# Performance work log

Measured on AMD Instinct MI355X. Metric: run time of the kernel, lower is better.

The kernel has to match this reference:

```python
import jax, jax.numpy as jnp
import numpy as np

EPS = 1e-5  # BatchNorm eps

B, LMAX = 64, 512
N_IN, N_OUT = 128, 256
LENGTHS = np.array([128 if i % 2 == 0 else 384 for i in range(B)], dtype=np.int64)  # sum = 16384
M = int(LENGTHS.sum())


def _bn(x, gamma, beta, mean, var):
    # eval-mode BatchNorm over channel (last) dim; x: [M, C]
    return (x - mean) * (gamma / jnp.sqrt(var + EPS)) + beta


def _aggregate(x, ld, am):
    # x: [M, N] ragged-concatenated node features; ld: [B] lengths; am: [B, L, L]
    # Equivalent to per-graph am[j,:l,:l] @ x_block, vectorized via zero-padding:
    # padded columns of am hit zero rows of x, and garbage rows are never gathered.
    Bn, L, _ = am.shape
    gid = jnp.repeat(jnp.arange(Bn), ld, total_repeat_length=x.shape[0])      # [M] graph id per node
    offs = jnp.concatenate([jnp.zeros((1,), ld.dtype), jnp.cumsum(ld)[:-1]])  # [B] start offsets
    pos = jnp.arange(x.shape[0]) - offs[gid]                                   # [M] within-graph position
    padded = jnp.zeros((Bn, L, x.shape[1]), x.dtype).at[gid, pos].set(x)       # [B, L, N]
    out = jnp.einsum('blm,bmn->bln', am, padded)                               # batched adjacency matmul
    return out[gid, pos]                                                       # back to ragged [M, N]


def setup_inputs() -> dict:
    key = jax.random.key(0)
    ks = jax.random.split(key, 12)
    x = jax.random.normal(ks[0], (M, N_IN, 1, 1), dtype=jnp.float32)
    ld = jnp.asarray(LENGTHS)
    am = jax.random.normal(ks[1], (B, LMAX, LMAX), dtype=jnp.float32)

    def lin_bn(kw, kb, cin, cout):
        W = jax.random.normal(kw, (cout, cin), dtype=jnp.float32) / np.sqrt(cin)
        b = jax.random.normal(kb, (cout,), dtype=jnp.float32) * 0.01
        kg, kbt, km, kv = jax.random.split(jax.random.fold_in(kw, 7), 4)
        gamma = 1.0 + 0.1 * jax.random.normal(kg, (cout,), dtype=jnp.float32)
        beta = 0.1 * jax.random.normal(kbt, (cout,), dtype=jnp.float32)
        mean = 0.1 * jax.random.normal(km, (cout,), dtype=jnp.float32)
        var = 0.5 + jax.random.uniform(kv, (cout,), dtype=jnp.float32)
        return W, b, gamma, beta, mean, var

    Wl, bl, gl, betal, ml, vl = lin_bn(ks[2], ks[3], N_IN, N_OUT)   # residual 1x1 conv + BN
    W1, b1, g1, beta1, m1, v1 = lin_bn(ks[4], ks[5], N_IN, N_IN)    # graph conv layer 1
    W2, b2, g2, beta2, m2, v2 = lin_bn(ks[6], ks[7], N_IN, N_OUT)   # graph conv layer 2
    return {
        'x': x, 'ld': ld, 'am': am,
        'Wl': Wl, 'bl': bl, 'gl': gl, 'betal': betal, 'ml': ml, 'vl': vl,
        'W1': W1, 'b1': b1, 'g1': g1, 'beta1': beta1, 'm1': m1, 'v1': v1,
        'W2': W2, 'b2': b2, 'g2': g2, 'beta2': beta2, 'm2': m2, 'v2': v2,
    }


def reference(x, ld, am,
              Wl, bl, gl, betal, ml, vl,
              W1, b1, g1, beta1, m1, v1,
              W2, b2, g2, beta2, m2, v2):
    xf = x.reshape(x.shape[0], x.shape[1])  # squeeze [M, N, 1, 1] -> [M, N]
    # residual branch (input_size != output_size): 1x1 conv + BN
    residual = _bn(xf @ Wl.T + bl, gl, betal, ml, vl)
    # graph conv layer 1: aggregate -> conv1x1 -> BN -> ReLU (dropout inactive in eval)
    h = _aggregate(xf, ld, am)
    h = jax.nn.relu(_bn(h @ W1.T + b1, g1, beta1, m1, v1))
    # graph conv layer 2: aggregate -> conv1x1 -> BN
    h = _aggregate(h, ld, am)
    h = _bn(h @ W2.T + b2, g2, beta2, m2, v2)
    out = jax.nn.leaky_relu(h + residual, negative_slope=0.01)
    return out[:, :, None, None]  # [M, N_out, 1, 1]
```

## Files before the change

kernel.cpp:

```cpp
#include <hip/hip_runtime.h>

#define EPS 1e-5f

typedef __attribute__((ext_vector_type(4))) float f32x4;
typedef __attribute__((ext_vector_type(8))) _Float16 f16x8;
typedef __attribute__((ext_vector_type(4))) _Float16 f16x4;

__device__ __forceinline__ int tidx(int r, int k, int K) {
    return (r >> 4) * (K << 4) + ((k >> 5) << 9) + ((r & 15) << 5) + (((k & 31) >> 3) << 3) + (k & 7);
}

#define MFMA16(a, b, c) __builtin_amdgcn_mfma_f32_16x16x32_f16(a, b, c, 0, 0, 0)

__device__ __forceinline__ void slot_map(int s, int& g, int& r0) {
    int c = s >> 6, j = s & 63;
    if (j < 48) { g = c * 8 + 2 * (j / 12) + 1; r0 = (j % 12) << 5; }
    else        { int jj = j - 48; g = c * 8 + 2 * (jj / 4); r0 = (jj % 4) << 5; }
}

__global__ __launch_bounds__(256) void prep_conv_kernel(
    const int* __restrict__ ld, const float* __restrict__ am,
    const float* __restrict__ Wl, const float* __restrict__ bl,
    const float* __restrict__ gl, const float* __restrict__ betal,
    const float* __restrict__ ml, const float* __restrict__ vl,
    const float* __restrict__ W1, const float* __restrict__ b1,
    const float* __restrict__ g1, const float* __restrict__ beta1,
    const float* __restrict__ m1, const float* __restrict__ v1,
    const float* __restrict__ W2, const float* __restrict__ b2,
    const float* __restrict__ g2, const float* __restrict__ beta2,
    const float* __restrict__ m2, const float* __restrict__ v2,
    int* __restrict__ offs, float* __restrict__ c1, float* __restrict__ cf,
    int* __restrict__ tg, int* __restrict__ tr, int* __restrict__ ta, int n_tasks,
    _Float16* __restrict__ W1t, _Float16* __restrict__ Wct,
    _Float16* __restrict__ amt,
    const float* __restrict__ x, _Float16* __restrict__ XTt,
    _Float16* __restrict__ xh_t, int M)
{
    __shared__ __align__(16) _Float16 Tt[128][80];
    int t = threadIdx.x;
    if (blockIdx.x < 256) {
        int m0 = blockIdx.x * 64;
        int gg = 0, off = 0;
        while (m0 >= off + ld[gg]) { off += ld[gg]; ++gg; }
        int l = ld[gg];
        #pragma unroll
        for (int p = 0; p < 8; ++p) {
            int idx = t + p * 256;
            int m = idx >> 5;
            int f = (idx & 31) * 4;
            float4 v = *(const float4*)&x[(size_t)(m0 + m) * 128 + f];
            Tt[f + 0][m] = (_Float16)v.x; Tt[f + 1][m] = (_Float16)v.y;
            Tt[f + 2][m] = (_Float16)v.z; Tt[f + 3][m] = (_Float16)v.w;
            f16x4 h;
            h[0] = (_Float16)v.x; h[1] = (_Float16)v.y;
            h[2] = (_Float16)v.z; h[3] = (_Float16)v.w;
            *(f16x4*)&xh_t[tidx(m0 + m, f, 128)] = h;
        }
        __syncthreads();
        #pragma unroll
        for (int p = 0; p < 4; ++p) {
            int idx = t + p * 256;
            int f = idx >> 3;
            int m8 = (idx & 7) * 8;
            int kl = m0 - off + m8;
            uint4 v = *(const uint4*)&Tt[f][m8];
            *(uint4*)&XTt[off * 128 + tidx(f, kl, l)] = v;
        }
    } else if (blockIdx.x < 320) {
        int b = blockIdx.x - 256;
        int gt = b * 256 + t;
        const int gsize = 64 * 256;
        if (b == 0) {
            if (t < 64) {
                int s = 0;
                for (int i = 0; i < t; ++i) s += ld[i];
                offs[t] = s;
            }
            if (t < 128) {
                float s1 = g1[t] * rsqrtf(v1[t] + EPS);
                c1[t] = (b1[t] - m1[t]) * s1 + beta1[t];
            }
            if (t < 256) {
                float s2 = g2[t] * rsqrtf(v2[t] + EPS);
                float sl = gl[t] * rsqrtf(vl[t] + EPS);
                cf[t] = (b2[t] - m2[t]) * s2 + beta2[t] + (bl[t] - ml[t]) * sl + betal[t];
            }
            for (int s = t; s < n_tasks; s += 256) {
                int g, r0;
                slot_map(s, g, r0);
                int amo = 0;
                for (int gg2 = 0; gg2 < g; ++gg2) { int L = ld[gg2]; amo += L * L; }
                tg[s] = g;
                tr[s] = r0;
                ta[s] = amo;
            }
        }
        for (int idx = gt; idx < 128 * 128; idx += gsize) {
            int n = idx >> 7, k = idx & 127;
            float s1 = g1[n] * rsqrtf(v1[n] + EPS);
            W1t[tidx(n, k, 128)] = (_Float16)(W1[idx] * s1);
        }
        for (int idx = gt; idx < 256 * 256; idx += gsize) {
            int n = idx >> 8, k = idx & 255;
            float v;
            if (k < 128) {
                float s2 = g2[n] * rsqrtf(v2[n] + EPS);
                v = W2[n * 128 + k] * s2;
            } else {
                float sl = gl[n] * rsqrtf(vl[n] + EPS);
                v = Wl[n * 128 + (k - 128)] * sl;
            }
            Wct[tidx(n, k, 256)] = (_Float16)v;
        }
    } else {
        int b2 = blockIdx.x - 320;
        int s = ((b2 & 7) << 6) + (b2 >> 3);
        int g, r0;
        slot_map(s, g, r0);
        int amo = 0;
        for (int gg2 = 0; gg2 < g; ++gg2) { int L = ld[gg2]; amo += L * L; }
        int l = ld[g];
        const float* src = am + (size_t)g * (512 * 512);
        _Float16* dst = amt + amo;
        int lq = l >> 2;
        int tot = lq << 5;
        for (int q = t; q < tot; q += 256) {
            int row = q / lq;
            int c4 = (q - row * lq) << 2;
            float4 v = *(const float4*)&src[(size_t)(r0 + row) * 512 + c4];
            f16x4 h;
            h[0] = (_Float16)v.x; h[1] = (_Float16)v.y;
            h[2] = (_Float16)v.z; h[3] = (_Float16)v.w;
            *(f16x4*)&dst[tidx(r0 + row, c4, l)] = h;
        }
    }
}

#define STAGED64()                                                            \
    {                                                                         \
        uint4 a0 = *(const uint4*)(sa);                                       \
        uint4 a1 = *(const uint4*)(sa + 512);                                 \
        uint4 b0v, b1v;                                                       \
        if (isB) { b0v = *(const uint4*)(sb); b1v = *(const uint4*)(sb + 512); } \
        *(uint4*)&Ast[0][dstA] = a0;                                          \
        *(uint4*)&Ast[0][4096 + dstA] = a1;                                   \
        if (isB) {                                                            \
            *(uint4*)&Bst[0][dstB] = b0v;                                     \
            *(uint4*)&Bst[0][1024 + dstB] = b1v;                              \
        }                                                                     \
        __syncthreads();                                                      \
        int cur = 0;                                                          \
        for (int s = 0; s < nk; s += 2) {                                     \
            uint4 na0, na1, nb0, nb1;                                         \
            if (s + 2 < nk) {                                                 \
                na0 = *(const uint4*)(sa + ((s + 2) << 9));                   \
                na1 = *(const uint4*)(sa + ((s + 3) << 9));                   \
                if (isB) {                                                    \
                    nb0 = *(const uint4*)(sb + ((s + 2) << 9));               \
                    nb1 = *(const uint4*)(sb + ((s + 3) << 9));               \
                }                                                             \
            }                                                                 \
            {                                                                 \
                f16x8 a   = *(const f16x8*)&Ast[cur][(w << 9) + rdo];         \
                f16x8 bb0 = *(const f16x8*)&Bst[cur][rdo];                    \
                f16x8 bb1 = *(const f16x8*)&Bst[cur][512 + rdo];              \
                acc0 = MFMA16(a, bb0, acc0);                                  \
                acc1 = MFMA16(a, bb1, acc1);                                  \
            }                                                                 \
            {                                                                 \
                f16x8 a   = *(const f16x8*)&Ast[cur][4096 + (w << 9) + rdo];  \
                f16x8 bb0 = *(const f16x8*)&Bst[cur][1024 + rdo];             \
                f16x8 bb1 = *(const f16x8*)&Bst[cur][1536 + rdo];             \
                acc0 = MFMA16(a, bb0, acc0);                                  \
                acc1 = MFMA16(a, bb1, acc1);                                  \
            }                                                                 \
            if (s + 2 < nk) {                                                 \
                int nxt = cur ^ 1;                                            \
                *(uint4*)&Ast[nxt][dstA] = na0;                               \
                *(uint4*)&Ast[nxt][4096 + dstA] = na1;                        \
                if (isB) {                                                    \
                    *(uint4*)&Bst[nxt][dstB] = nb0;                           \
                    *(uint4*)&Bst[nxt][1024 + dstB] = nb1;                    \
                }                                                             \
                __syncthreads();                                              \
                cur = nxt;                                                    \
            }                                                                 \
        }                                                                     \
    }

__global__ __launch_bounds__(512) void fused1s_kernel(
    const _Float16* __restrict__ amt, const _Float16* __restrict__ XTt,
    const int* __restrict__ ld, const int* __restrict__ offs,
    const int* __restrict__ tg, const int* __restrict__ tr, const int* __restrict__ ta,
    const _Float16* __restrict__ W1t, const float* __restrict__ bias,
    _Float16* __restrict__ H2Tt)
{
    int task = ((blockIdx.x & 7) << 6) + (blockIdx.x >> 3);
    int g = tg[task];
    int l = ld[g];
    int off = offs[g];

    int tid = threadIdx.x;
    int lane = tid & 63;
    int w = tid >> 6;
    int l15 = lane & 15;
    int l4 = lane >> 4;

    __shared__ __align__(16) _Float16 Ast[2][8192];
    __shared__ __align__(16) _Float16 Bst[2][2048];
    __shared__ __align__(16) _Float16 Hs[32][136];

    const int ts = l << 4;
    const int nk = l >> 5;
    const int lane_off = (l15 << 5) + (l4 << 3);
    const int rdo = lane_off ^ ((l15 & 7) << 3);

    int idx63 = tid & 63;
    int wr = idx63 >> 2, wc = idx63 & 3;
    int wt = (wr << 5) + (wc << 3);
    int wts = wt ^ ((wr & 7) << 3);
    const int dstA = ((tid >> 6) << 9) + wts;
    const int dstB = (((tid >> 6) & 1) << 9) + wts;
    const bool isB = tid < 128;

    const _Float16* sa = XTt + off * 128 + (tid >> 6) * ts + (idx63 << 3);
    const _Float16* sb = amt + ta[task]
        + ((tr[task] >> 4) + ((tid >> 6) & 1)) * ts + (idx63 << 3);

    f32x4 acc0 = {0.f, 0.f, 0.f, 0.f}, acc1 = acc0;
    STAGED64()

    {
        f16x4 o0, o1;
        #pragma unroll
        for (int r = 0; r < 4; ++r) { o0[r] = (_Float16)acc0[r]; o1[r] = (_Float16)acc1[r]; }
        *(f16x4*)&Hs[l15][w * 16 + (l4 << 2)] = o0;
        *(f16x4*)&Hs[16 + l15][w * 16 + (l4 << 2)] = o1;
    }
    __syncthreads();

    const _Float16* wbase = W1t + w * 2048 + lane_off;
    f32x4 e0 = {0.f, 0.f, 0.f, 0.f}, e1 = e0;
    #pragma unroll
    for (int s = 0; s < 4; ++s) {
        int ho = (s << 5) + (l4 << 3);
        f16x8 a0 = *(const f16x8*)&Hs[l15][ho];
        f16x8 a1 = *(const f16x8*)&Hs[16 + l15][ho];
        f16x8 b  = *(const f16x8*)(wbase + (s << 9));
        e0 = MFMA16(a0, b, e0);
        e1 = MFMA16(a1, b, e1);
    }
    int hb = off * 128;
    int trb = tr[task];
    int n = w * 16 + l15;
    float bv = bias[n];
    {
        f16x4 o;
        #pragma unroll
        for (int r = 0; r < 4; ++r) {
            float v = e0[r] + bv;
            o[r] = (_Float16)(v > 0.f ? v : 0.f);
        }
        *(f16x4*)&H2Tt[hb + tidx(n, trb + (l4 << 2), l)] = o;
    }
    {
        f16x4 o;
        #pragma unroll
        for (int r = 0; r < 4; ++r) {
            float v = e1[r] + bv;
            o[r] = (_Float16)(v > 0.f ? v : 0.f);
        }
        *(f16x4*)&H2Tt[hb + tidx(n, trb + 16 + (l4 << 2), l)] = o;
    }
}

__global__ __launch_bounds__(512) void fused2s_kernel(
    const _Float16* __restrict__ amt, const _Float16* __restrict__ H2Tt,
    const int* __restrict__ ld, const int* __restrict__ offs,
    const int* __restrict__ tg, const int* __restrict__ tr, const int* __restrict__ ta,
    const _Float16* __restrict__ xh_t, const _Float16* __restrict__ Wct,
    const float* __restrict__ bias, float* __restrict__ out)
{
    int task = ((blockIdx.x & 7) << 6) + (blockIdx.x >> 3);
    int g = tg[task];
    int l = ld[g];
    int off = offs[g];

    int tid = threadIdx.x;
    int lane = tid & 63;
    int w = tid >> 6;
    int l15 = lane & 15;
    int l4 = lane >> 4;

    __shared__ __align__(16) _Float16 Ast[2][8192];
    __shared__ __align__(16) _Float16 Bst[2][2048];
    __shared__ __align__(16) _Float16 Hs[32][136];

    const int ts = l << 4;
    const int nk = l >> 5;
    const int lane_off = (l15 << 5) + (l4 << 3);
    const int rdo = lane_off ^ ((l15 & 7) << 3);

    int idx63 = tid & 63;
    int wr = idx63 >> 2, wc = idx63 & 3;
    int wt = (wr << 5) + (wc << 3);
    int wts = wt ^ ((wr & 7) << 3);
    const int dstA = ((tid >> 6) << 9) + wts;
    const int dstB = (((tid >> 6) & 1) << 9) + wts;
    const bool isB = tid < 128;

    const _Float16* sa = H2Tt + off * 128 + (tid >> 6) * ts + (idx63 << 3);
    const _Float16* sb = amt + ta[task]
        + ((tr[task] >> 4) + ((tid >> 6) & 1)) * ts + (idx63 << 3);

    f32x4 acc0 = {0.f, 0.f, 0.f, 0.f}, acc1 = acc0;
    STAGED64()

    {
        f16x4 o0, o1;
        #pragma unroll
        for (int r = 0; r < 4; ++r) { o0[r] = (_Float16)acc0[r]; o1[r] = (_Float16)acc1[r]; }
        *(f16x4*)&Hs[l15][w * 16 + (l4 << 2)] = o0;
        *(f16x4*)&Hs[16 + l15][w * 16 + (l4 << 2)] = o1;
    }
    __syncthreads();

    int gmb = off + tr[task];
    const _Float16* wb0 = Wct + (w * 2) * 4096 + lane_off;
    const _Float16* wb1 = wb0 + 4096;
    const _Float16* xp0 = xh_t + (gmb >> 4) * 2048 + lane_off;
    const _Float16* xp1 = xp0 + 2048;
    f32x4 e00 = {0.f, 0.f, 0.f, 0.f}, e01 = e00, e10 = e00, e11 = e00;
    #pragma unroll
    for (int s = 0; s < 8; ++s) {
        f16x8 a0, a1;
        if (s < 4) {
            int ho = (s << 5) + (l4 << 3);
            a0 = *(const f16x8*)&Hs[l15][ho];
            a1 = *(const f16x8*)&Hs[16 + l15][ho];
        } else {
            a0 = *(const f16x8*)(xp0 + ((s - 4) << 9));
            a1 = *(const f16x8*)(xp1 + ((s - 4) << 9));
        }
        f16x8 b0 = *(const f16x8*)(wb0 + (s << 9));
        f16x8 b1 = *(const f16x8*)(wb1 + (s << 9));
        e00 = MFMA16(a0, b0, e00);
        e01 = MFMA16(a1, b0, e01);
        e10 = MFMA16(a0, b1, e10);
        e11 = MFMA16(a1, b1, e11);
    }
    int n0 = w * 32 + l15;
    int n1 = n0 + 16;
    float bv0 = bias[n0], bv1 = bias[n1];
    #pragma unroll
    for (int r = 0; r < 4; ++r) {
        int m0r = gmb + (l4 << 2) + r;
        int m1r = m0r + 16;
        float v;
        v = e00[r] + bv0; out[(size_t)m0r * 256 + n0] = v > 0.f ? v : 0.01f * v;
        v = e01[r] + bv0; out[(size_t)m1r * 256 + n0] = v > 0.f ? v : 0.01f * v;
        v = e10[r] + bv1; out[(size_t)m0r * 256 + n1] = v > 0.f ? v : 0.01f * v;
        v = e11[r] + bv1; out[(size_t)m1r * 256 + n1] = v > 0.f ? v : 0.01f * v;
    }
}

extern "C" void kernel_launch(void* const* d_in, const int* in_sizes, int n_in,
                              void* d_out, int out_size, void* d_ws, size_t ws_size,
                              hipStream_t stream) {
    const float* x     = (const float*)d_in[0];
    const int*   ld    = (const int*)d_in[1];
    const float* am    = (const float*)d_in[2];
    const float* Wl    = (const float*)d_in[3];
    const float* bl    = (const float*)d_in[4];
    const float* gl    = (const float*)d_in[5];
    const float* betal = (const float*)d_in[6];
    const float* ml    = (const float*)d_in[7];
    const float* vl    = (const float*)d_in[8];
    const float* W1    = (const float*)d_in[9];
    const float* b1    = (const float*)d_in[10];
    const float* g1    = (const float*)d_in[11];
    const float* beta1 = (const float*)d_in[12];
    const float* m1    = (const float*)d_in[13];
    const float* v1    = (const float*)d_in[14];
    const float* W2    = (const float*)d_in[15];
    const float* b2    = (const float*)d_in[16];
    const float* g2    = (const float*)d_in[17];
    const float* beta2 = (const float*)d_in[18];
    const float* m2    = (const float*)d_in[19];
    const float* v2    = (const float*)d_in[20];
    float* out = (float*)d_out;

    int M = in_sizes[0] / 128;
    int n_tasks = M / 32;

    char* w = (char*)d_ws;
    int*   offs = (int*)(w);
    float* c1   = (float*)(w + 512);
    float* cf   = (float*)(w + 1024);
    int*   tg   = (int*)(w + 2048);
    int*   tr   = (int*)(w + 4096);
    int*   ta   = (int*)(w + 6144);
    _Float16* W1t = (_Float16*)(w + 16384);
    _Float16* Wct = (_Float16*)(w + 49152);
    _Float16* amt = (_Float16*)(w + 180224);
    _Float16* XTt = (_Float16*)(w + 180224 + (size_t)10485760);
    _Float16* xh_t = XTt + (size_t)M * 128;
    _Float16* H2Tt = xh_t + (size_t)M * 128;

    prep_conv_kernel<<<832, 256, 0, stream>>>(ld, am,
        Wl, bl, gl, betal, ml, vl,
        W1, b1, g1, beta1, m1, v1,
        W2, b2, g2, beta2, m2, v2,
        offs, c1, cf, tg, tr, ta, n_tasks, W1t, Wct, amt, x, XTt, xh_t, M);

    fused1s_kernel<<<n_tasks, 512, 0, stream>>>(amt, XTt, ld, offs, tg, tr, ta, W1t, c1, H2Tt);

    fused2s_kernel<<<n_tasks, 512, 0, stream>>>(amt, H2Tt, ld, offs, tg, tr, ta, xh_t, Wct, cf, out);
}
```

Before: 36.69 us.

## Stage GEMM tiles with direct global-to-LDS loads and pre-swizzled global layout

Replaces the register round-trip staging (global load into VGPRs, then LDS store) in both fused aggregation kernels with global_load_lds DMA transfers. To keep the bank-conflict-avoiding XOR swizzle without a per-thread scatter, the prep kernel and the layer-1 output now write XTt, amt and H2Tt in a pre-swizzled tiled layout (stidx). This is meant to cut VGPR pressure and LDS write instructions in the double-buffered K loop. In exchange it adds an extra barrier after the loop and relies on DMA-to-LDS completion ordering being covered by __syncthreads.

```diff
diff --git a/kernel.cpp b/kernel.cpp
--- a/kernel.cpp
+++ b/kernel.cpp
@@ -9,8 +9,18 @@
 __device__ __forceinline__ int tidx(int r, int k, int K) {
     return (r >> 4) * (K << 4) + ((k >> 5) << 9) + ((r & 15) << 5) + (((k & 31) >> 3) << 3) + (k & 7);
 }
+__device__ __forceinline__ int stidx(int r, int k, int K) {
+    int o = ((r & 15) << 5) + (((k & 31) >> 3) << 3) + (k & 7);
+    return (r >> 4) * (K << 4) + ((k >> 5) << 9) + (o ^ ((r & 7) << 3));
+}
 
 #define MFMA16(a, b, c) __builtin_amdgcn_mfma_f32_16x16x32_f16(a, b, c, 0, 0, 0)
+
+__device__ __forceinline__ void gload16(const _Float16* g, _Float16* l) {
+    __builtin_amdgcn_global_load_lds(
+        (const __attribute__((address_space(1))) void*)g,
+        (__attribute__((address_space(3))) void*)l, 16, 0, 0);
+}
 
 __device__ __forceinline__ void slot_map(int s, int& g, int& r0) {
     int c = s >> 6, j = s & 63;
@@ -64,7 +74,7 @@
             int m8 = (idx & 7) * 8;
             int kl = m0 - off + m8;
             uint4 v = *(const uint4*)&Tt[f][m8];
-            *(uint4*)&XTt[off * 128 + tidx(f, kl, l)] = v;
+            *(uint4*)&XTt[off * 128 + stidx(f, kl, l)] = v;
         }
     } else if (blockIdx.x < 320) {
         int b = blockIdx.x - 256;
@@ -131,60 +141,43 @@
             f16x4 h;
             h[0] = (_Float16)v.x; h[1] = (_Float16)v.y;
             h[2] = (_Float16)v.z; h[3] = (_Float16)v.w;
-            *(f16x4*)&dst[tidx(r0 + row, c4, l)] = h;
-        }
-    }
-}
-
-#define STAGED64()                                                            \
+            *(f16x4*)&dst[stidx(r0 + row, c4, l)] = h;
+        }
+    }
+}
+
+#define STAGE_BUF(B, S)                                                       \
     {                                                                         \
-        uint4 a0 = *(const uint4*)(sa);                                       \
-        uint4 a1 = *(const uint4*)(sa + 512);                                 \
-        uint4 b0v, b1v;                                                       \
-        if (isB) { b0v = *(const uint4*)(sb); b1v = *(const uint4*)(sb + 512); } \
-        *(uint4*)&Ast[0][dstA] = a0;                                          \
-        *(uint4*)&Ast[0][4096 + dstA] = a1;                                   \
-        if (isB) {                                                            \
-            *(uint4*)&Bst[0][dstB] = b0v;                                     \
-            *(uint4*)&Bst[0][1024 + dstB] = b1v;                              \
-        }                                                                     \
+        gload16(saw + ((S) << 9),       &Ast[B][(w << 9)]);                   \
+        gload16(saw + ((S + 1) << 9),   &Ast[B][4096 + (w << 9)]);            \
+        if (w < 4)                                                            \
+            gload16(sbw + (((S) + (w >> 1)) << 9),                            \
+                    &Bst[B][((w >> 1) << 10) + ((w & 1) << 9)]);              \
+    }
+
+#define COMPUTE_BUF(B)                                                        \
+    {                                                                         \
+        f16x8 a0  = *(const f16x8*)&Ast[B][(w << 9) + rdo];                   \
+        f16x8 bb0 = *(const f16x8*)&Bst[B][rdo];                              \
+        f16x8 bb1 = *(const f16x8*)&Bst[B][512 + rdo];                        \
+        acc0 = MFMA16(a0, bb0, acc0);                                         \
+        acc1 = MFMA16(a0, bb1, acc1);                                         \
+        f16x8 a1  = *(const f16x8*)&Ast[B][4096 + (w << 9) + rdo];            \
+        f16x8 bb2 = *(const f16x8*)&Bst[B][1024 + rdo];                       \
+        f16x8 bb3 = *(const f16x8*)&Bst[B][1536 + rdo];                       \
+        acc0 = MFMA16(a1, bb2, acc0);                                         \
+        acc1 = MFMA16(a1, bb3, acc1);                                         \
+    }
+
+#define STAGED64DMA()                                                         \
+    {                                                                         \
+        STAGE_BUF(0, 0)                                                       \
         __syncthreads();                                                      \
         int cur = 0;                                                          \
         for (int s = 0; s < nk; s += 2) {                                     \
-            uint4 na0, na1, nb0, nb1;                                         \
-            if (s + 2 < nk) {                                                 \
-                na0 = *(const uint4*)(sa + ((s + 2) << 9));                   \
-                na1 = *(const uint4*)(sa + ((s + 3) << 9));                   \
-                if (isB) {                                                    \
-                    nb0 = *(const uint4*)(sb + ((s + 2) << 9));               \
-                    nb1 = *(const uint4*)(sb + ((s + 3) << 9));               \
-                }                                                             \
-            }                                                                 \
-            {                                                                 \
-                f16x8 a   = *(const f16x8*)&Ast[cur][(w << 9) + rdo];         \
-                f16x8 bb0 = *(const f16x8*)&Bst[cur][rdo];                    \
-                f16x8 bb1 = *(const f16x8*)&Bst[cur][512 + rdo];              \
-                acc0 = MFMA16(a, bb0, acc0);                                  \
-                acc1 = MFMA16(a, bb1, acc1);                                  \
-            }                                                                 \
-            {                                                                 \
-                f16x8 a   = *(const f16x8*)&Ast[cur][4096 + (w << 9) + rdo];  \
-                f16x8 bb0 = *(const f16x8*)&Bst[cur][1024 + rdo];             \
-                f16x8 bb1 = *(const f16x8*)&Bst[cur][1536 + rdo];             \
-                acc0 = MFMA16(a, bb0, acc0);                                  \
-                acc1 = MFMA16(a, bb1, acc1);                                  \
-            }                                                                 \
-            if (s + 2 < nk) {                                                 \
-                int nxt = cur ^ 1;                                            \
-                *(uint4*)&Ast[nxt][dstA] = na0;                               \
-                *(uint4*)&Ast[nxt][4096 + dstA] = na1;                        \
-                if (isB) {                                                    \
-                    *(uint4*)&Bst[nxt][dstB] = nb0;                           \
-                    *(uint4*)&Bst[nxt][1024 + dstB] = nb1;                    \
-                }                                                             \
-                __syncthreads();                                              \
-                cur = nxt;                                                    \
-            }                                                                 \
+            if (s + 2 < nk) STAGE_BUF(cur ^ 1, s + 2)                         \
+            COMPUTE_BUF(cur)                                                  \
+            if (s + 2 < nk) { __syncthreads(); cur ^= 1; }                    \
         }                                                                     \
     }
 
@@ -215,21 +208,13 @@
     const int lane_off = (l15 << 5) + (l4 << 3);
     const int rdo = lane_off ^ ((l15 & 7) << 3);
 
-    int idx63 = tid & 63;
-    int wr = idx63 >> 2, wc = idx63 & 3;
-    int wt = (wr << 5) + (wc << 3);
-    int wts = wt ^ ((wr & 7) << 3);
-    const int dstA = ((tid >> 6) << 9) + wts;
-    const int dstB = (((tid >> 6) & 1) << 9) + wts;
-    const bool isB = tid < 128;
-
-    const _Float16* sa = XTt + off * 128 + (tid >> 6) * ts + (idx63 << 3);
-    const _Float16* sb = amt + ta[task]
-        + ((tr[task] >> 4) + ((tid >> 6) & 1)) * ts + (idx63 << 3);
+    const _Float16* saw = XTt + off * 128 + w * ts + (lane << 3);
+    const _Float16* sbw = amt + ta[task] + ((tr[task] >> 4) + (w & 1)) * ts + (lane << 3);
 
     f32x4 acc0 = {0.f, 0.f, 0.f, 0.f}, acc1 = acc0;
-    STAGED64()
-
+    STAGED64DMA()
+
+    __syncthreads();
     {
         f16x4 o0, o1;
         #pragma unroll
@@ -261,7 +246,7 @@
             float v = e0[r] + bv;
             o[r] = (_Float16)(v > 0.f ? v : 0.f);
         }
-        *(f16x4*)&H2Tt[hb + tidx(n, trb + (l4 << 2), l)] = o;
+        *(f16x4*)&H2Tt[hb + stidx(n, trb + (l4 << 2), l)] = o;
     }
     {
         f16x4 o;
@@ -270,7 +255,7 @@
             float v = e1[r] + bv;
             o[r] = (_Float16)(v > 0.f ? v : 0.f);
         }
-        *(f16x4*)&H2Tt[hb + tidx(n, trb + 16 + (l4 << 2), l)] = o;
+        *(f16x4*)&H2Tt[hb + stidx(n, trb + 16 + (l4 << 2), l)] = o;
     }
 }
 
@@ -301,21 +286,13 @@
     const int lane_off = (l15 << 5) + (l4 << 3);
     const int rdo = lane_off ^ ((l15 & 7) << 3);
 
-    int idx63 = tid & 63;
-    int wr = idx63 >> 2, wc = idx63 & 3;
-    int wt = (wr << 5) + (wc << 3);
-    int wts = wt ^ ((wr & 7) << 3);
-    const int dstA = ((tid >> 6) << 9) + wts;
-    const int dstB = (((tid >> 6) & 1) << 9) + wts;
-    const bool isB = tid < 128;
-
-    const _Float16* sa = H2Tt + off * 128 + (tid >> 6) * ts + (idx63 << 3);
-    const _Float16* sb = amt + ta[task]
-        + ((tr[task] >> 4) + ((tid >> 6) & 1)) * ts + (idx63 << 3);
+    const _Float16* saw = H2Tt + off * 128 + w * ts + (lane << 3);
+    const _Float16* sbw = amt + ta[task] + ((tr[task] >> 4) + (w & 1)) * ts + (lane << 3);
 
     f32x4 acc0 = {0.f, 0.f, 0.f, 0.f}, acc1 = acc0;
-    STAGED64()
-
+    STAGED64DMA()
+
+    __syncthreads();
     {
         f16x4 o0, o1;
         #pragma unroll
```

After: 37.59 us. 2.5% more time.
